# Kernel tuning notes

Measured on AMD Instinct MI355X. Metric: run time of the kernel, lower is better.

Reference implementation:

```python
import jax, jax.numpy as jnp
import numpy as np
import math

B, L, D_MODEL = 2, 2048, 1024
N_HEADS, D_HEAD = 16, 64
ROPE_BASE = 10000.0
PERIODS = (24, 168)
LAMBDAS = (0.5, 0.25)
NEG_INF = jnp.float32(-jnp.inf)


def _alibi_slopes(n_heads):
    # n_heads is a power of two here (16), so only the simple branch is needed
    start = 2.0 ** (-2.0 ** (-(math.log2(n_heads) - 3)))
    return jnp.asarray([start * (start ** i) for i in range(n_heads)], dtype=jnp.float32)


def _apply_rope(x, cos_t, sin_t):
    # x: [B,H,L,Dh]; cos_t/sin_t: [1,1,L,Dh//2]
    x1, x2 = x[..., 0::2], x[..., 1::2]
    xr1 = x1 * cos_t - x2 * sin_t
    xr2 = x1 * sin_t + x2 * cos_t
    return jnp.stack([xr1, xr2], axis=-1).reshape(x.shape)


def setup_inputs() -> dict:
    key = jax.random.key(0)
    ks = jax.random.split(key, 5)
    d = D_MODEL
    return {
        "x": jax.random.normal(ks[0], (B, L, d), dtype=jnp.float32),
        "Wq": jax.random.normal(ks[1], (d, d), dtype=jnp.float32) * 0.02,
        "bq": jnp.zeros((d,), dtype=jnp.float32),
        "Wk": jax.random.normal(ks[2], (d, d), dtype=jnp.float32) * 0.02,
        "bk": jnp.zeros((d,), dtype=jnp.float32),
        "Wv": jax.random.normal(ks[3], (d, d), dtype=jnp.float32) * 0.02,
        "bv": jnp.zeros((d,), dtype=jnp.float32),
        "Wo": jax.random.normal(ks[4], (d, d), dtype=jnp.float32) * 0.02,
        "bo": jnp.zeros((d,), dtype=jnp.float32),
    }


def reference(x, Wq, bq, Wk, bk, Wv, bv, Wo, bo):
    Bn, Ln, Dn = x.shape
    H, Dh = N_HEADS, D_HEAD

    def proj(W, b):
        return (x @ W + b).reshape(Bn, Ln, H, Dh).transpose(0, 2, 1, 3)  # [B,H,L,Dh]

    q, k, v = proj(Wq, bq), proj(Wk, bk), proj(Wv, bv)

    # RoPE angles: theta[l, m] = l / base^(2m/Dh)
    inv = 1.0 / (ROPE_BASE ** (jnp.arange(0, Dh, 2, dtype=jnp.float32) / Dh))
    theta = jnp.arange(Ln, dtype=jnp.float32)[:, None] * inv[None, :]  # [L, Dh/2]
    cos_t = jnp.cos(theta)[None, None]
    sin_t = jnp.sin(theta)[None, None]
    q = _apply_rope(q, cos_t, sin_t)
    k = _apply_rope(k, cos_t, sin_t)

    scale = 1.0 / math.sqrt(Dh)
    attn = jnp.einsum("bhid,bhjd->bhij", q, k) * scale  # [B,H,L,L]

    i = jnp.arange(Ln)[:, None]
    j = jnp.arange(Ln)[None, :]

    # ALiBi bias: -slope * relu(j - i), per head
    slopes = _alibi_slopes(H)  # [H]
    dist = (j - i).astype(jnp.float32)
    attn = attn + (-slopes[None, :, None, None]) * jax.nn.relu(dist)[None, None]

    # periodic cosine bias
    d_abs = jnp.abs(dist)
    pb = jnp.zeros_like(d_abs)
    for P, lam in zip(PERIODS, LAMBDAS):
        pb = pb + lam * jnp.cos(2.0 * math.pi * d_abs / float(P))
    attn = attn + pb[None, None]

    # causal mask (torch: attn + full(-inf).triu(1))
    attn = jnp.where((j > i)[None, None], NEG_INF, attn)

    p = jax.nn.softmax(attn, axis=-1)  # dropout=0 -> identity
    out = jnp.einsum("bhij,bhjd->bhid", p, v)
    out = out.transpose(0, 2, 1, 3).reshape(Bn, Ln, Dn)
    return out @ Wo + bo, p
```

## Files before the change

kernel.cpp:

```cpp
#include <hip/hip_runtime.h>
#include <math.h>

#define B_  2
#define L_  2048
#define D_  1024
#define H_  16
#define DH_ 64
#define BL_ (B_*L_)

typedef unsigned short u16;
typedef __attribute__((ext_vector_type(8))) short short8;
typedef __attribute__((ext_vector_type(4))) float f32x4;
typedef __attribute__((ext_vector_type(4))) unsigned short u16x4;

template<bool V> struct BC { static constexpr bool value = V; };

#define WS_XB   0
#define WS_WT4  2097152
#define WS_QB   4194304
#define WS_KB   6291456
#define WS_VT   8388608
#define WS_AOB  10485760
#define WS_COS  12582912
#define WS_SIN  12648448
#define WS_PBL  12713984

__device__ __forceinline__ u16 f2b(float f) {
  union { float f; unsigned u; } v; v.f = f;
  unsigned r = (v.u + 0x7fffu + ((v.u >> 16) & 1u)) >> 16;
  return (u16)r;
}
__device__ __forceinline__ u16x4 f2b4(float a, float b, float c, float d) {
  u16x4 u; u.x = f2b(a); u.y = f2b(b); u.z = f2b(c); u.w = f2b(d); return u;
}
__device__ __forceinline__ float bf2f(u16 u) {
  union { unsigned u; float f; } v; v.u = ((unsigned)u) << 16; return v.f;
}
__device__ __forceinline__ void gl_lds16(const void* g, void* l) {
  __builtin_amdgcn_global_load_lds(
      (const __attribute__((address_space(1))) unsigned int*)g,
      (__attribute__((address_space(3))) unsigned int*)l, 16, 0, 0);
}
__device__ __forceinline__ void nt_store4(float x, float y, float z, float w, float* p) {
  f32x4 v = (f32x4){x, y, z, w};
  __builtin_nontemporal_store(v, (f32x4*)p);
}

__global__ void fill_tables(float* __restrict__ costab, float* __restrict__ sintab,
                            float* __restrict__ pbl) {
  int idx = blockIdx.x * 256 + threadIdx.x;
  if (idx < L_ * 32) {
    int l = idx >> 5, tp = idx & 31;
    double inv = pow(10000.0, -2.0 * (double)tp / 64.0);
    double th  = (double)l * inv;
    costab[idx] = (float)cos(th);
    sintab[idx] = (float)sin(th);
  }
  if (idx < L_) {
    double d = (double)idx;
    double v = 0.5  * cos(6.283185307179586 * d / 24.0)
             + 0.25 * cos(6.283185307179586 * d / 168.0);
    pbl[idx] = (float)(v * 1.4426950408889634);
  }
}

__global__ __launch_bounds__(256) void xcast(const float* __restrict__ x, u16* __restrict__ xb) {
  const size_t i = ((size_t)blockIdx.x * 256 + threadIdx.x) * 8;
  float4 a = *(const float4*)(x + i);
  float4 b = *(const float4*)(x + i + 4);
  u16 us[8] = { f2b(a.x),f2b(a.y),f2b(a.z),f2b(a.w), f2b(b.x),f2b(b.y),f2b(b.z),f2b(b.w) };
  *(short8*)(xb + i) = *(short8*)us;
}

__global__ __launch_bounds__(256) void wtrans4(const float* __restrict__ W0, const float* __restrict__ W1,
                                               const float* __restrict__ W2, const float* __restrict__ W3,
                                               u16* __restrict__ Wt) {
  __shared__ u16 tt[64][80];
  const int z = blockIdx.z;
  const float* W = (z == 0) ? W0 : (z == 1) ? W1 : (z == 2) ? W2 : W3;
  u16* Wtz = Wt + (size_t)z * 1024 * 1024;
  const int k0 = blockIdx.x << 6, n0 = blockIdx.y << 6;
  const int t = threadIdx.x;
  {
    const int r = t >> 4, c4 = (t & 15) << 2;
    for (int rr = r; rr < 64; rr += 16) {
      float4 v = *(const float4*)(W + (size_t)(k0 + rr) * D_ + n0 + c4);
      tt[c4+0][rr] = f2b(v.x); tt[c4+1][rr] = f2b(v.y);
      tt[c4+2][rr] = f2b(v.z); tt[c4+3][rr] = f2b(v.w);
    }
  }
  __syncthreads();
  const int n = t >> 2, kc = (t & 3) << 4;
  u16* dst = Wtz + (size_t)(n0 + n) * D_ + k0 + kc;
  #pragma unroll
  for (int u = 0; u < 16; ++u) dst[u] = tt[n][kc + u];
}

template<int KIND>
__global__ __launch_bounds__(256) void gemm_k(
    const u16* __restrict__ Ag, const u16* __restrict__ Bg,
    const float* __restrict__ b0, const float* __restrict__ b1, const float* __restrict__ b2,
    const float* __restrict__ costab, const float* __restrict__ sintab,
    u16* __restrict__ O0, u16* __restrict__ O1, u16* __restrict__ O2,
    float* __restrict__ Cout)
{
  __shared__ u16 As[8192];
  __shared__ u16 Bs[8192];
  const int t = threadIdx.x, w = t >> 6, lane = t & 63;
  const int lt = lane & 15, lg = lane >> 4;
  const int wg = blockIdx.x + (blockIdx.y << 5);
  int sid;
  if constexpr (KIND == 1) sid = (wg & 7) * 96 + (wg >> 3);
  else                     sid = (wg & 7) * 32 + (wg >> 3);
  const int row0 = (sid & 31) << 7;
  const int gy   = sid >> 5;
  const int col0 = gy << 7;
  const int wm = (w & 1) << 6, wn = (w >> 1) << 6;
  const int proj = (KIND == 1) ? (gy >> 3) : 0;
  const bool swp = (KIND == 0) || (proj < 2);

  const int srow = lane >> 3;
  const int gch  = (lane & 7) ^ (srow & 7);
  const u16* aptr[4]; const u16* bptr[4];
  char* adst[4]; char* bdst[4];
  #pragma unroll
  for (int u = 0; u < 4; ++u) {
    const int rl = w * 32 + u * 8 + srow;
    aptr[u] = Ag + (size_t)(row0 + rl) * 1024 + gch * 8;
    bptr[u] = Bg + (size_t)(col0 + rl) * 1024 + gch * 8;
    adst[u] = (char*)As + (w * 32 + u * 8) * 128;
    bdst[u] = (char*)Bs + (w * 32 + u * 8) * 128;
  }
  int aoff[2][4], boff[2][4];
  #pragma unroll
  for (int ks = 0; ks < 2; ++ks)
    #pragma unroll
    for (int q = 0; q < 4; ++q) {
      const int ra = wm + q * 16 + lt;
      aoff[ks][q] = ra * 128 + (((ks * 4 + lg) ^ (ra & 7)) << 4);
      const int rb = wn + q * 16 + lt;
      boff[ks][q] = rb * 128 + (((ks * 4 + lg) ^ (rb & 7)) << 4);
    }

  f32x4 acc[4][4];
  #pragma unroll
  for (int i = 0; i < 4; ++i)
    #pragma unroll
    for (int j = 0; j < 4; ++j) acc[i][j] = (f32x4){0.f,0.f,0.f,0.f};

  auto loop = [&](auto SW) {
    for (int kt = 0; kt < 16; ++kt) {
      #pragma unroll
      for (int u = 0; u < 4; ++u) {
        gl_lds16(aptr[u] + kt * 64, adst[u]);
        gl_lds16(bptr[u] + kt * 64, bdst[u]);
      }
      __syncthreads();
      #pragma unroll
      for (int ks = 0; ks < 2; ++ks) {
        short8 af[4], bf[4];
        #pragma unroll
        for (int q = 0; q < 4; ++q) {
          af[q] = *(const short8*)((const char*)As + aoff[ks][q]);
          bf[q] = *(const short8*)((const char*)Bs + boff[ks][q]);
        }
        #pragma unroll
        for (int mi = 0; mi < 4; ++mi)
          #pragma unroll
          for (int nj = 0; nj < 4; ++nj) {
            if constexpr (decltype(SW)::value)
              acc[mi][nj] = __builtin_amdgcn_mfma_f32_16x16x32_bf16(bf[nj], af[mi], acc[mi][nj], 0, 0, 0);
            else
              acc[mi][nj] = __builtin_amdgcn_mfma_f32_16x16x32_bf16(af[mi], bf[nj], acc[mi][nj], 0, 0, 0);
          }
      }
      __syncthreads();
    }
  };
  if (swp) loop(BC<true>{}); else loop(BC<false>{});

  if constexpr (KIND == 0) {
    #pragma unroll
    for (int mi = 0; mi < 4; ++mi) {
      const int m = row0 + wm + mi * 16 + lt;
      #pragma unroll
      for (int nj = 0; nj < 4; ++nj) {
        const int nb = col0 + wn + nj * 16 + (lg << 2);
        float4 bb = *(const float4*)(b0 + nb);
        nt_store4(acc[mi][nj][0] + bb.x, acc[mi][nj][1] + bb.y,
                  acc[mi][nj][2] + bb.z, acc[mi][nj][3] + bb.w,
                  Cout + (size_t)m * 1024 + nb);
      }
    }
  } else if (proj < 2) {
    const float* bias = proj ? b1 : b0;
    u16* Ob = proj ? O1 : O0;
    const int col0p = (gy & 7) << 7;
    #pragma unroll
    for (int mi = 0; mi < 4; ++mi) {
      const int m = row0 + wm + mi * 16 + lt;
      const int bb_ = m >> 11, lpos = m & (L_ - 1);
      #pragma unroll
      for (int nj = 0; nj < 4; ++nj) {
        const int nb = col0p + wn + nj * 16 + (lg << 2);
        const int d0 = nb & 63, h = nb >> 6;
        float4 ba = *(const float4*)(bias + nb);
        const float o0 = acc[mi][nj][0] + ba.x, o1 = acc[mi][nj][1] + ba.y;
        const float o2 = acc[mi][nj][2] + ba.z, o3 = acc[mi][nj][3] + ba.w;
        const float* ct = costab + lpos * 32 + (d0 >> 1);
        const float* st = sintab + lpos * 32 + (d0 >> 1);
        const float c0 = ct[0], c1 = ct[1], s0 = st[0], s1 = st[1];
        const float r0 = o0 * c0 - o1 * s0, r1 = o0 * s0 + o1 * c0;
        const float r2 = o2 * c1 - o3 * s1, r3 = o2 * s1 + o3 * c1;
        *(u16x4*)(Ob + ((size_t)(bb_ * 16 + h) * L_ + lpos) * 64 + d0) = f2b4(r0, r1, r2, r3);
      }
    }
  } else {
    const int col0p = (gy & 7) << 7;
    #pragma unroll
    for (int mi = 0; mi < 4; ++mi) {
      const int lb = row0 + wm + mi * 16 + (lg << 2);
      const int bb_ = lb >> 11;
      #pragma unroll
      for (int nj = 0; nj < 4; ++nj) {
        const int n = col0p + wn + nj * 16 + lt;
        const int h = n >> 6, dh = n & 63;
        const float bv1 = b2[n];
        *(u16x4*)(O2 + ((size_t)(bb_ * 16 + h) * 64 + dh) * L_ + (lb & (L_ - 1))) =
            f2b4(acc[mi][nj][0] + bv1, acc[mi][nj][1] + bv1,
                 acc[mi][nj][2] + bv1, acc[mi][nj][3] + bv1);
      }
    }
  }
}

__global__ __launch_bounds__(512, 4) void attn_mfma(
    const u16* __restrict__ Qb, const u16* __restrict__ Kb, const u16* __restrict__ Vt,
    const float* __restrict__ pbg, float* __restrict__ Pout, u16* __restrict__ AOb)
{
  __shared__ u16 PL[33 * 16 * 64];
  __shared__ float PVacc[2][16][64];
  __shared__ float lsbuf[8][2][16];
  float* pbl = &PVacc[0][0][0];
  const int t = threadIdx.x, w = t >> 6, lane = t & 63;
  const int lt = lane & 15, lg = lane >> 4;
  *(float4*)(pbl + t * 4) = *(const float4*)(pbg + t * 4);
  const int wg = blockIdx.x + (blockIdx.y << 6);
  const int sid = (wg & 7) * 256 + (wg >> 3);
  const int bh = sid >> 6, pr = sid & 63;
  const int b = bh >> 4, h = bh & 15;
  const int sA = pr, sB = 127 - pr;
  const int kvA = (sA >> 2) + 1, kvB = (sB >> 2) + 1;
  const int swz = (lt & 7) << 4;
  const float C1 = 0.18033688011112042f;
  char* PLb = (char*)PL;
  __syncthreads();

  f32x4 oaccA[4], oaccB[4];
  #pragma unroll
  for (int dt = 0; dt < 4; ++dt) {
    oaccA[dt] = (f32x4){0.f,0.f,0.f,0.f};
    oaccB[dt] = (f32x4){0.f,0.f,0.f,0.f};
  }
  float lsumA = 0.f, lsumB = 0.f;

  auto tile = [&](int s, int kvt, const short8& q0, const short8& q1,
                  f32x4* oacc, float& lsum, int pb0, int rstride, bool masked) {
    const int j0 = kvt << 6;
    const int i  = s * 16 + lt;
    const u16* kp = Kb + ((size_t)bh * L_ + j0 + lt) * 64 + lg * 8;
    short8 kf[8];
    #pragma unroll
    for (int jt = 0; jt < 4; ++jt) {
      kf[2*jt]   = *(const short8*)(kp + jt * 1024);
      kf[2*jt+1] = *(const short8*)(kp + jt * 1024 + 32);
    }
    f32x4 z[4];
    #pragma unroll
    for (int jt = 0; jt < 4; ++jt) {
      f32x4 zz = (f32x4){0.f,0.f,0.f,0.f};
      zz = __builtin_amdgcn_mfma_f32_16x16x32_bf16(kf[2*jt],   q0, zz, 0, 0, 0);
      zz = __builtin_amdgcn_mfma_f32_16x16x32_bf16(kf[2*jt+1], q1, zz, 0, 0, 0);
      z[jt] = zz;
    }
    const u16* vp = Vt + ((size_t)bh * 64 + lt) * L_ + j0 + lg * 8;
    short8 vf[8];
    #pragma unroll
    for (int dt = 0; dt < 4; ++dt) {
      vf[2*dt]   = *(const short8*)(vp + dt * 16 * L_);
      vf[2*dt+1] = *(const short8*)(vp + dt * 16 * L_ + 32);
    }
    #pragma unroll
    for (int jt = 0; jt < 4; ++jt) {
      const int jb = j0 + jt * 16 + (lg << 2);
      const int dd = i - jb;
      float pr4[4];
      if (masked) {
        #pragma unroll
        for (int r = 0; r < 4; ++r) {
          const int d  = dd - r;
          const int dc = d < 0 ? 0 : d;
          const float pe = exp2f(fmaf(z[jt][r], C1, pbl[dc]));
          pr4[r] = d < 0 ? 0.f : pe;
          lsum += pr4[r];
        }
      } else {
        #pragma unroll
        for (int r = 0; r < 4; ++r) {
          pr4[r] = exp2f(fmaf(z[jt][r], C1, pbl[dd - r]));
          lsum += pr4[r];
        }
      }
      *(u16x4*)(PLb + pb0 + lt * rstride + ((kvt * 128 + jt * 32 + lg * 8) ^ swz)) =
          f2b4(pr4[0], pr4[1], pr4[2], pr4[3]);
    }
    short8 pa0 = *(const short8*)(PLb + pb0 + lt * rstride + ((kvt * 128 + lg * 16) ^ swz));
    short8 pa1 = *(const short8*)(PLb + pb0 + lt * rstride + ((kvt * 128 + 64 + lg * 16) ^ swz));
    #pragma unroll
    for (int dt = 0; dt < 4; ++dt) {
      oacc[dt] = __builtin_amdgcn_mfma_f32_16x16x32_bf16(pa0, vf[2*dt],   oacc[dt], 0, 0, 0);
      oacc[dt] = __builtin_amdgcn_mfma_f32_16x16x32_bf16(pa1, vf[2*dt+1], oacc[dt], 0, 0, 0);
    }
  };

  {
    const u16* qpA = Qb + ((size_t)bh * L_ + sA * 16 + lt) * 64 + lg * 8;
    const short8 qA0 = *(const short8*)(qpA), qA1 = *(const short8*)(qpA + 32);
    for (int kvt = w; kvt < kvA; kvt += 8)
      tile(sA, kvt, qA0, qA1, oaccA, lsumA, 0, kvA << 7, kvt == kvA - 1);
  }
  lsumA += __shfl_xor(lsumA, 16); lsumA += __shfl_xor(lsumA, 32);
  if (lane < 16) lsbuf[w][0][lt] = lsumA;
  __syncthreads();

  float rvA[2]; const char* rbA[2]; float* prowA[2]; int limA[2], rswA[2];
  #pragma unroll
  for (int u = 0; u < 2; ++u) {
    const int rl = w * 2 + u;
    float den = 0.f;
    #pragma unroll
    for (int ww = 0; ww < 8; ++ww) den += lsbuf[ww][0][rl];
    rvA[u] = 1.f / den;
    rbA[u] = PLb + rl * (kvA << 7);
    rswA[u] = (rl & 7) << 4;
    const int i = sA * 16 + rl;
    limA[u] = i >> 2;
    prowA[u] = Pout + ((size_t)bh * L_ + i) * L_;
  }
  int chunk = 0;
  auto storeA = [&](int c) {
    const int u = c >> 3, cc = c & 7;
    const int c4 = lane + cc * 64;
    float ox = 0.f, oy = 0.f, oz = 0.f, ow = 0.f;
    if (c4 <= limA[u]) {
      u16x4 dv = *(const u16x4*)(rbA[u] + ((c4 << 3) ^ rswA[u]));
      const float rv = rvA[u];
      ox = bf2f(dv.x) * rv; oy = bf2f(dv.y) * rv;
      oz = bf2f(dv.z) * rv; ow = bf2f(dv.w) * rv;
      if (c4 == limA[u]) {
        const int i = sA * 16 + (w * 2 + u);
        const int j0c = c4 << 2;
        if (j0c + 1 > i) oy = 0.f;
        if (j0c + 2 > i) oz = 0.f;
        if (j0c + 3 > i) ow = 0.f;
      }
    }
    nt_store4(ox, oy, oz, ow, prowA[u] + (c4 << 2));
  };

  {
    const u16* qpB = Qb + ((size_t)bh * L_ + sB * 16 + lt) * 64 + lg * 8;
    const short8 qB0 = *(const short8*)(qpB), qB1 = *(const short8*)(qpB + 32);
    const int pb0 = kvA << 11, rstride = kvB << 7;
    const int iB = sB * 16 + lt;
    for (int kvt = w; kvt < kvB; kvt += 8) {
      const bool masked = (kvt == kvB - 1);
      const int j0 = kvt << 6;
      const u16* kp = Kb + ((size_t)bh * L_ + j0 + lt) * 64 + lg * 8;
      short8 kf[8];
      #pragma unroll
      for (int jt = 0; jt < 4; ++jt) {
        kf[2*jt]   = *(const short8*)(kp + jt * 1024);
        kf[2*jt+1] = *(const short8*)(kp + jt * 1024 + 32);
      }
      f32x4 z[4];
      #pragma unroll
      for (int jt = 0; jt < 4; ++jt) {
        f32x4 zz = (f32x4){0.f,0.f,0.f,0.f};
        zz = __builtin_amdgcn_mfma_f32_16x16x32_bf16(kf[2*jt],   qB0, zz, 0, 0, 0);
        zz = __builtin_amdgcn_mfma_f32_16x16x32_bf16(kf[2*jt+1], qB1, zz, 0, 0, 0);
        z[jt] = zz;
      }
      const u16* vp = Vt + ((size_t)bh * 64 + lt) * L_ + j0 + lg * 8;
      short8 vf[8];
      #pragma unroll
      for (int dt = 0; dt < 4; ++dt) {
        vf[2*dt]   = *(const short8*)(vp + dt * 16 * L_);
        vf[2*dt+1] = *(const short8*)(vp + dt * 16 * L_ + 32);
      }
      {
        const int lim = (chunk + 6 < 16) ? chunk + 6 : 16;
        for (; chunk < lim; ++chunk) storeA(chunk);
      }
      #pragma unroll
      for (int jt = 0; jt < 4; ++jt) {
        const int jb = j0 + jt * 16 + (lg << 2);
        const int dd = iB - jb;
        float pr4[4];
        if (masked) {
          #pragma unroll
          for (int r = 0; r < 4; ++r) {
            const int d  = dd - r;
            const int dc = d < 0 ? 0 : d;
            const float pe = exp2f(fmaf(z[jt][r], C1, pbl[dc]));
            pr4[r] = d < 0 ? 0.f : pe;
            lsumB += pr4[r];
          }
        } else {
          #pragma unroll
          for (int r = 0; r < 4; ++r) {
            pr4[r] = exp2f(fmaf(z[jt][r], C1, pbl[dd - r]));
            lsumB += pr4[r];
          }
        }
        *(u16x4*)(PLb + pb0 + lt * rstride + ((kvt * 128 + jt * 32 + lg * 8) ^ swz)) =
            f2b4(pr4[0], pr4[1], pr4[2], pr4[3]);
      }
      short8 pa0 = *(const short8*)(PLb + pb0 + lt * rstride + ((kvt * 128 + lg * 16) ^ swz));
      short8 pa1 = *(const short8*)(PLb + pb0 + lt * rstride + ((kvt * 128 + 64 + lg * 16) ^ swz));
      #pragma unroll
      for (int dt = 0; dt < 4; ++dt) {
        oaccB[dt] = __builtin_amdgcn_mfma_f32_16x16x32_bf16(pa0, vf[2*dt],   oaccB[dt], 0, 0, 0);
        oaccB[dt] = __builtin_amdgcn_mfma_f32_16x16x32_bf16(pa1, vf[2*dt+1], oaccB[dt], 0, 0, 0);
      }
    }
    for (; chunk < 16; ++chunk) storeA(chunk);
  }

  lsumB += __shfl_xor(lsumB, 16); lsumB += __shfl_xor(lsumB, 32);
  if (lane < 16) lsbuf[w][1][lt] = lsumB;
  __syncthreads();
  {
    #pragma unroll
    for (int u = 0; u < 2; ++u) {
      const int rl = w * 2 + u;
      float den = 0.f;
      #pragma unroll
      for (int ww = 0; ww < 8; ++ww) den += lsbuf[ww][1][rl];
      const float rv = 1.f / den;
      const char* rb = PLb + (kvA << 11) + rl * (kvB << 7);
      const int rsw = (rl & 7) << 4;
      const int i = sB * 16 + rl;
      float* prow = Pout + ((size_t)bh * L_ + i) * L_;
      const int lim4 = i >> 2;
      #pragma unroll
      for (int cc = 0; cc < 8; ++cc) {
        const int c4 = lane + cc * 64;
        float ox = 0.f, oy = 0.f, oz = 0.f, ow = 0.f;
        if (c4 <= lim4) {
          u16x4 dv = *(const u16x4*)(rb + ((c4 << 3) ^ rsw));
          ox = bf2f(dv.x) * rv; oy = bf2f(dv.y) * rv;
          oz = bf2f(dv.z) * rv; ow = bf2f(dv.w) * rv;
          if (c4 == lim4) {
            const int j0c = c4 << 2;
            if (j0c + 1 > i) oy = 0.f;
            if (j0c + 2 > i) oz = 0.f;
            if (j0c + 3 > i) ow = 0.f;
          }
        }
        nt_store4(ox, oy, oz, ow, prow + (c4 << 2));
      }
    }
  }

  for (int rr = 0; rr < 8; ++rr) {
    if (w == rr) {
      #pragma unroll
      for (int dt = 0; dt < 4; ++dt)
        #pragma unroll
        for (int r = 0; r < 4; ++r) {
          if (rr == 0) {
            PVacc[0][(lg << 2) + r][dt * 16 + lt] = oaccA[dt][r];
            PVacc[1][(lg << 2) + r][dt * 16 + lt] = oaccB[dt][r];
          } else {
            PVacc[0][(lg << 2) + r][dt * 16 + lt] += oaccA[dt][r];
            PVacc[1][(lg << 2) + r][dt * 16 + lt] += oaccB[dt][r];
          }
        }
    }
    __syncthreads();
  }
  {
    const int st = t >> 8, rl = (t >> 4) & 15, c0 = (t & 15) << 2;
    float den = 0.f;
    #pragma unroll
    for (int ww = 0; ww < 8; ++ww) den += lsbuf[ww][st][rl];
    const float rv = 1.f / den;
    const int s_ = st ? sB : sA;
    const int i = s_ * 16 + rl;
    u16x4 o = f2b4(PVacc[st][rl][c0] * rv, PVacc[st][rl][c0 + 1] * rv,
                   PVacc[st][rl][c0 + 2] * rv, PVacc[st][rl][c0 + 3] * rv);
    *(u16x4*)(AOb + ((size_t)(b * L_ + i)) * 1024 + h * 64 + c0) = o;
  }
}

extern "C" void kernel_launch(void* const* d_in, const int* in_sizes, int n_in,
                              void* d_out, int out_size, void* d_ws, size_t ws_size,
                              hipStream_t stream) {
  const float* x  = (const float*)d_in[0];
  const float* Wq = (const float*)d_in[1];
  const float* bq = (const float*)d_in[2];
  const float* Wk = (const float*)d_in[3];
  const float* bk = (const float*)d_in[4];
  const float* Wv = (const float*)d_in[5];
  const float* bv = (const float*)d_in[6];
  const float* Wo = (const float*)d_in[7];
  const float* bo = (const float*)d_in[8];

  float* out  = (float*)d_out;
  float* Pout = out + (size_t)BL_ * D_;

  float* ws = (float*)d_ws;
  u16* XB  = (u16*)(ws + WS_XB);
  u16* WT4 = (u16*)(ws + WS_WT4);
  u16* QB  = (u16*)(ws + WS_QB);
  u16* KB  = (u16*)(ws + WS_KB);
  u16* VT  = (u16*)(ws + WS_VT);
  u16* AOB = (u16*)(ws + WS_AOB);
  float* cosT = ws + WS_COS;
  float* sinT = ws + WS_SIN;
  float* pblG = ws + WS_PBL;

  fill_tables<<<256, 256, 0, stream>>>(cosT, sinT, pblG);
  xcast<<<2048, 256, 0, stream>>>(x, XB);
  wtrans4<<<dim3(16,16,4), 256, 0, stream>>>(Wq, Wk, Wv, Wo, WT4);

  gemm_k<1><<<dim3(32,24), 256, 0, stream>>>(XB, WT4, bq, bk, bv, cosT, sinT,
                                             QB, KB, VT, nullptr);

  attn_mfma<<<dim3(64,32), 512, 0, stream>>>(QB, KB, VT, pblG, Pout, AOB);

  gemm_k<0><<<dim3(32,8), 256, 0, stream>>>(AOB, WT4 + (size_t)3*1024*1024, bo,
                                            nullptr, nullptr, nullptr, nullptr,
                                            nullptr, nullptr, nullptr, out);
}
```

Before: 292.7 us.

## Merge prep kernels, remap QKV GEMM tile order, restructure attention P stores

The three preprocessing kernels (bf16 cast of x, weight transpose, RoPE and periodic-bias tables) are merged into one launch, with branches chosen by block index, to cut launch overhead and serialization gaps. The QKV GEMM block-to-tile mapping is changed so each XCD gets consecutive row tiles within a projection group, aiming for better L2 reuse. In attention, the first segment's softmax-probability rows are now written out in the first two iterations of the second segment's loop instead of spread in chunks of six. The second segment's rows are assigned to warps as rp*8+w instead of w*2+u. The A-row stores are only correct if every warp runs at least two iterations of the second loop.

```diff
diff --git a/kernel.cpp b/kernel.cpp
--- a/kernel.cpp
+++ b/kernel.cpp
@@ -46,54 +46,57 @@
   __builtin_nontemporal_store(v, (f32x4*)p);
 }
 
-__global__ void fill_tables(float* __restrict__ costab, float* __restrict__ sintab,
-                            float* __restrict__ pbl) {
-  int idx = blockIdx.x * 256 + threadIdx.x;
-  if (idx < L_ * 32) {
-    int l = idx >> 5, tp = idx & 31;
-    double inv = pow(10000.0, -2.0 * (double)tp / 64.0);
-    double th  = (double)l * inv;
-    costab[idx] = (float)cos(th);
-    sintab[idx] = (float)sin(th);
-  }
-  if (idx < L_) {
-    double d = (double)idx;
-    double v = 0.5  * cos(6.283185307179586 * d / 24.0)
-             + 0.25 * cos(6.283185307179586 * d / 168.0);
-    pbl[idx] = (float)(v * 1.4426950408889634);
-  }
-}
-
-__global__ __launch_bounds__(256) void xcast(const float* __restrict__ x, u16* __restrict__ xb) {
-  const size_t i = ((size_t)blockIdx.x * 256 + threadIdx.x) * 8;
-  float4 a = *(const float4*)(x + i);
-  float4 b = *(const float4*)(x + i + 4);
-  u16 us[8] = { f2b(a.x),f2b(a.y),f2b(a.z),f2b(a.w), f2b(b.x),f2b(b.y),f2b(b.z),f2b(b.w) };
-  *(short8*)(xb + i) = *(short8*)us;
-}
-
-__global__ __launch_bounds__(256) void wtrans4(const float* __restrict__ W0, const float* __restrict__ W1,
-                                               const float* __restrict__ W2, const float* __restrict__ W3,
-                                               u16* __restrict__ Wt) {
+__global__ __launch_bounds__(256) void prep(
+    const float* __restrict__ x, u16* __restrict__ xb,
+    const float* __restrict__ W0, const float* __restrict__ W1,
+    const float* __restrict__ W2, const float* __restrict__ W3,
+    u16* __restrict__ Wt,
+    float* __restrict__ costab, float* __restrict__ sintab, float* __restrict__ pbl)
+{
   __shared__ u16 tt[64][80];
-  const int z = blockIdx.z;
-  const float* W = (z == 0) ? W0 : (z == 1) ? W1 : (z == 2) ? W2 : W3;
-  u16* Wtz = Wt + (size_t)z * 1024 * 1024;
-  const int k0 = blockIdx.x << 6, n0 = blockIdx.y << 6;
+  const int blk = blockIdx.x;
   const int t = threadIdx.x;
-  {
-    const int r = t >> 4, c4 = (t & 15) << 2;
-    for (int rr = r; rr < 64; rr += 16) {
-      float4 v = *(const float4*)(W + (size_t)(k0 + rr) * D_ + n0 + c4);
-      tt[c4+0][rr] = f2b(v.x); tt[c4+1][rr] = f2b(v.y);
-      tt[c4+2][rr] = f2b(v.z); tt[c4+3][rr] = f2b(v.w);
-    }
-  }
-  __syncthreads();
-  const int n = t >> 2, kc = (t & 3) << 4;
-  u16* dst = Wtz + (size_t)(n0 + n) * D_ + k0 + kc;
-  #pragma unroll
-  for (int u = 0; u < 16; ++u) dst[u] = tt[n][kc + u];
+  if (blk < 2048) {
+    const size_t i = ((size_t)blk * 256 + t) * 8;
+    float4 a = *(const float4*)(x + i);
+    float4 b = *(const float4*)(x + i + 4);
+    u16 us[8] = { f2b(a.x),f2b(a.y),f2b(a.z),f2b(a.w), f2b(b.x),f2b(b.y),f2b(b.z),f2b(b.w) };
+    *(short8*)(xb + i) = *(short8*)us;
+  } else if (blk < 3072) {
+    const int r2 = blk - 2048;
+    const int z = r2 >> 8, rem = r2 & 255;
+    const float* W = (z == 0) ? W0 : (z == 1) ? W1 : (z == 2) ? W2 : W3;
+    u16* Wtz = Wt + (size_t)z * 1024 * 1024;
+    const int k0 = (rem & 15) << 6, n0 = (rem >> 4) << 6;
+    {
+      const int r = t >> 4, c4 = (t & 15) << 2;
+      for (int rr = r; rr < 64; rr += 16) {
+        float4 v = *(const float4*)(W + (size_t)(k0 + rr) * D_ + n0 + c4);
+        tt[c4+0][rr] = f2b(v.x); tt[c4+1][rr] = f2b(v.y);
+        tt[c4+2][rr] = f2b(v.z); tt[c4+3][rr] = f2b(v.w);
+      }
+    }
+    __syncthreads();
+    const int n = t >> 2, kc = (t & 3) << 4;
+    u16* dst = Wtz + (size_t)(n0 + n) * D_ + k0 + kc;
+    #pragma unroll
+    for (int u = 0; u < 16; ++u) dst[u] = tt[n][kc + u];
+  } else {
+    const int idx = (blk - 3072) * 256 + t;
+    if (idx < L_ * 32) {
+      int l = idx >> 5, tp = idx & 31;
+      double inv = pow(10000.0, -2.0 * (double)tp / 64.0);
+      double th  = (double)l * inv;
+      costab[idx] = (float)cos(th);
+      sintab[idx] = (float)sin(th);
+    }
+    if (idx < L_) {
+      double d = (double)idx;
+      double v = 0.5  * cos(6.283185307179586 * d / 24.0)
+               + 0.25 * cos(6.283185307179586 * d / 168.0);
+      pbl[idx] = (float)(v * 1.4426950408889634);
+    }
+  }
 }
 
 template<int KIND>
@@ -110,8 +113,13 @@
   const int lt = lane & 15, lg = lane >> 4;
   const int wg = blockIdx.x + (blockIdx.y << 5);
   int sid;
-  if constexpr (KIND == 1) sid = (wg & 7) * 96 + (wg >> 3);
-  else                     sid = (wg & 7) * 32 + (wg >> 3);
+  if constexpr (KIND == 1) {
+    const int xcd = wg & 7, q = wg >> 3;
+    const int bx = q / 3, g3 = q - bx * 3;
+    sid = (xcd * 3 + g3) * 32 + bx;
+  } else {
+    sid = (wg & 7) * 32 + (wg >> 3);
+  }
   const int row0 = (sid & 31) << 7;
   const int gy   = sid >> 5;
   const int col0 = gy << 7;
@@ -333,47 +341,26 @@
   if (lane < 16) lsbuf[w][0][lt] = lsumA;
   __syncthreads();
 
-  float rvA[2]; const char* rbA[2]; float* prowA[2]; int limA[2], rswA[2];
+  const int rA0 = w * 2, rA1 = rA0 + 1;
+  float den0 = 0.f, den1 = 0.f;
   #pragma unroll
-  for (int u = 0; u < 2; ++u) {
-    const int rl = w * 2 + u;
-    float den = 0.f;
-    #pragma unroll
-    for (int ww = 0; ww < 8; ++ww) den += lsbuf[ww][0][rl];
-    rvA[u] = 1.f / den;
-    rbA[u] = PLb + rl * (kvA << 7);
-    rswA[u] = (rl & 7) << 4;
-    const int i = sA * 16 + rl;
-    limA[u] = i >> 2;
-    prowA[u] = Pout + ((size_t)bh * L_ + i) * L_;
-  }
-  int chunk = 0;
-  auto storeA = [&](int c) {
-    const int u = c >> 3, cc = c & 7;
-    const int c4 = lane + cc * 64;
-    float ox = 0.f, oy = 0.f, oz = 0.f, ow = 0.f;
-    if (c4 <= limA[u]) {
-      u16x4 dv = *(const u16x4*)(rbA[u] + ((c4 << 3) ^ rswA[u]));
-      const float rv = rvA[u];
-      ox = bf2f(dv.x) * rv; oy = bf2f(dv.y) * rv;
-      oz = bf2f(dv.z) * rv; ow = bf2f(dv.w) * rv;
-      if (c4 == limA[u]) {
-        const int i = sA * 16 + (w * 2 + u);
-        const int j0c = c4 << 2;
-        if (j0c + 1 > i) oy = 0.f;
-        if (j0c + 2 > i) oz = 0.f;
-        if (j0c + 3 > i) ow = 0.f;
-      }
-    }
-    nt_store4(ox, oy, oz, ow, prowA[u] + (c4 << 2));
-  };
+  for (int ww = 0; ww < 8; ++ww) { den0 += lsbuf[ww][0][rA0]; den1 += lsbuf[ww][0][rA1]; }
+  const float rv0 = 1.f / den0, rv1 = 1.f / den1;
+  const char* rb0 = PLb + rA0 * (kvA << 7);
+  const char* rb1 = PLb + rA1 * (kvA << 7);
+  const int sw0 = (rA0 & 7) << 4, sw1 = (rA1 & 7) << 4;
+  const int iA0 = sA * 16 + rA0, iA1 = sA * 16 + rA1;
+  const int lim0 = iA0 >> 2, lim1 = iA1 >> 2;
+  float* prow0 = Pout + ((size_t)bh * L_ + iA0) * L_;
+  float* prow1 = Pout + ((size_t)bh * L_ + iA1) * L_;
 
   {
     const u16* qpB = Qb + ((size_t)bh * L_ + sB * 16 + lt) * 64 + lg * 8;
     const short8 qB0 = *(const short8*)(qpB), qB1 = *(const short8*)(qpB + 32);
     const int pb0 = kvA << 11, rstride = kvB << 7;
     const int iB = sB * 16 + lt;
-    for (int kvt = w; kvt < kvB; kvt += 8) {
+    int itc = 0;
+    for (int kvt = w; kvt < kvB; kvt += 8, ++itc) {
       const bool masked = (kvt == kvB - 1);
       const int j0 = kvt << 6;
       const u16* kp = Kb + ((size_t)bh * L_ + j0 + lt) * 64 + lg * 8;
@@ -398,9 +385,42 @@
         vf[2*dt]   = *(const short8*)(vp + dt * 16 * L_);
         vf[2*dt+1] = *(const short8*)(vp + dt * 16 * L_ + 32);
       }
-      {
-        const int lim = (chunk + 6 < 16) ? chunk + 6 : 16;
-        for (; chunk < lim; ++chunk) storeA(chunk);
+      if (itc == 0) {
+        #pragma unroll
+        for (int cc = 0; cc < 8; ++cc) {
+          const int c4 = lane + cc * 64;
+          float ox = 0.f, oy = 0.f, oz = 0.f, ow = 0.f;
+          if (c4 <= lim0) {
+            u16x4 dv = *(const u16x4*)(rb0 + ((c4 << 3) ^ sw0));
+            ox = bf2f(dv.x) * rv0; oy = bf2f(dv.y) * rv0;
+            oz = bf2f(dv.z) * rv0; ow = bf2f(dv.w) * rv0;
+            if (c4 == lim0) {
+              const int j0c = c4 << 2;
+              if (j0c + 1 > iA0) oy = 0.f;
+              if (j0c + 2 > iA0) oz = 0.f;
+              if (j0c + 3 > iA0) ow = 0.f;
+            }
+          }
+          nt_store4(ox, oy, oz, ow, prow0 + (c4 << 2));
+        }
+      } else if (itc == 1) {
+        #pragma unroll
+        for (int cc = 0; cc < 8; ++cc) {
+          const int c4 = lane + cc * 64;
+          float ox = 0.f, oy = 0.f, oz = 0.f, ow = 0.f;
+          if (c4 <= lim1) {
+            u16x4 dv = *(const u16x4*)(rb1 + ((c4 << 3) ^ sw1));
+            ox = bf2f(dv.x) * rv1; oy = bf2f(dv.y) * rv1;
+            oz = bf2f(dv.z) * rv1; ow = bf2f(dv.w) * rv1;
+            if (c4 == lim1) {
+              const int j0c = c4 << 2;
+              if (j0c + 1 > iA1) oy = 0.f;
+              if (j0c + 2 > iA1) oz = 0.f;
+              if (j0c + 3 > iA1) ow = 0.f;
+            }
+          }
+          nt_store4(ox, oy, oz, ow, prow1 + (c4 << 2));
+        }
       }
       #pragma unroll
       for (int jt = 0; jt < 4; ++jt) {
@@ -434,42 +454,39 @@
         oaccB[dt] = __builtin_amdgcn_mfma_f32_16x16x32_bf16(pa1, vf[2*dt+1], oaccB[dt], 0, 0, 0);
       }
     }
-    for (; chunk < 16; ++chunk) storeA(chunk);
   }
 
   lsumB += __shfl_xor(lsumB, 16); lsumB += __shfl_xor(lsumB, 32);
   if (lane < 16) lsbuf[w][1][lt] = lsumB;
   __syncthreads();
-  {
-    #pragma unroll
-    for (int u = 0; u < 2; ++u) {
-      const int rl = w * 2 + u;
-      float den = 0.f;
-      #pragma unroll
-      for (int ww = 0; ww < 8; ++ww) den += lsbuf[ww][1][rl];
-      const float rv = 1.f / den;
-      const char* rb = PLb + (kvA << 11) + rl * (kvB << 7);
-      const int rsw = (rl & 7) << 4;
-      const int i = sB * 16 + rl;
-      float* prow = Pout + ((size_t)bh * L_ + i) * L_;
-      const int lim4 = i >> 2;
-      #pragma unroll
-      for (int cc = 0; cc < 8; ++cc) {
-        const int c4 = lane + cc * 64;
-        float ox = 0.f, oy = 0.f, oz = 0.f, ow = 0.f;
-        if (c4 <= lim4) {
-          u16x4 dv = *(const u16x4*)(rb + ((c4 << 3) ^ rsw));
-          ox = bf2f(dv.x) * rv; oy = bf2f(dv.y) * rv;
-          oz = bf2f(dv.z) * rv; ow = bf2f(dv.w) * rv;
-          if (c4 == lim4) {
-            const int j0c = c4 << 2;
-            if (j0c + 1 > i) oy = 0.f;
-            if (j0c + 2 > i) oz = 0.f;
-            if (j0c + 3 > i) ow = 0.f;
-          }
-        }
-        nt_store4(ox, oy, oz, ow, prow + (c4 << 2));
-      }
+  #pragma unroll
+  for (int rp = 0; rp < 2; ++rp) {
+    const int rl = rp * 8 + w;
+    const int i  = sB * 16 + rl;
+    float den = 0.f;
+    #pragma unroll
+    for (int ww = 0; ww < 8; ++ww) den += lsbuf[ww][1][rl];
+    const float rv = 1.f / den;
+    const char* rb = PLb + (kvA << 11) + rl * (kvB << 7);
+    const int rsw = (rl & 7) << 4;
+    float* prow = Pout + ((size_t)bh * L_ + i) * L_;
+    const int lim4 = i >> 2;
+    #pragma unroll
+    for (int cc = 0; cc < 8; ++cc) {
+      const int c4 = lane + cc * 64;
+      float ox = 0.f, oy = 0.f, oz = 0.f, ow = 0.f;
+      if (c4 <= lim4) {
+        u16x4 dv = *(const u16x4*)(rb + ((c4 << 3) ^ rsw));
+        ox = bf2f(dv.x) * rv; oy = bf2f(dv.y) * rv;
+        oz = bf2f(dv.z) * rv; ow = bf2f(dv.w) * rv;
+        if (c4 == lim4) {
+          const int j0c = c4 << 2;
+          if (j0c + 1 > i) oy = 0.f;
+          if (j0c + 2 > i) oz = 0.f;
+          if (j0c + 3 > i) ow = 0.f;
+        }
+      }
+      nt_store4(ox, oy, oz, ow, prow + (c4 << 2));
     }
   }
 
@@ -531,9 +548,7 @@
   float* sinT = ws + WS_SIN;
   float* pblG = ws + WS_PBL;
 
-  fill_tables<<<256, 256, 0, stream>>>(cosT, sinT, pblG);
-  xcast<<<2048, 256, 0, stream>>>(x, XB);
-  wtrans4<<<dim3(16,16,4), 256, 0, stream>>>(Wq, Wk, Wv, Wo, WT4);
+  prep<<<3328, 256, 0, stream>>>(x, XB, Wq, Wk, Wv, Wo, WT4, cosT, sinT, pblG);
 
   gemm_k<1><<<dim3(32,24), 256, 0, stream>>>(XB, WT4, bq, bk, bv, cosT, sinT,
                                              QB, KB, VT, nullptr);
```

Result: slower. 310.0 us (+5.9%).
